# Performance work log

Measured on AMD Instinct MI355X. Metric: run time of the kernel, lower is better.

## Reference

```python
import jax, jax.numpy as jnp
import numpy as np

MARGIN = 0.3
EPS = 0.1              # label smoothing weight
NUM_CLASSES = 100000
WEIGHT_T = 1.0
WEIGHT_X = 1.0
BATCH = 1024
EMBED_DIM = 512


def setup_inputs() -> dict:
    key = jax.random.key(0)
    k1, k2, k3 = jax.random.split(key, 3)
    x = jax.random.normal(k1, (BATCH, EMBED_DIM), dtype=jnp.float32)
    # classifier: weight ~ N(0, 0.01), bias = 0 (matches nn.init in module)
    W = jax.random.normal(k2, (NUM_CLASSES, EMBED_DIM), dtype=jnp.float32) * 0.01
    b = jnp.zeros((NUM_CLASSES,), dtype=jnp.float32)
    labels = jax.random.randint(k3, (BATCH,), 0, NUM_CLASSES)
    return {"x": x, "W": W, "b": b, "labels": labels}


def reference(x, W, b, labels):
    # ---- TripletLoss with batch-hard mining ----
    sq = jnp.sum(x * x, axis=1)                      # [B]
    dist = sq[:, None] + sq[None, :] - 2.0 * (x @ x.T)  # [B, B]
    dist = jnp.sqrt(jnp.clip(dist, 1e-12))
    same = labels[:, None] == labels[None, :]        # [B, B] (diagonal True)
    dist_ap = jnp.max(jnp.where(same, dist, -jnp.inf), axis=1)  # hardest positive
    dist_an = jnp.min(jnp.where(same, jnp.inf, dist), axis=1)   # hardest negative
    # MarginRankingLoss(dist_an, dist_ap, y=1) = mean(relu(dist_ap - dist_an + margin))
    triplet_loss = jnp.mean(jnp.maximum(dist_ap - dist_an + MARGIN, 0.0))

    # ---- CrossEntropy with label smoothing ----
    logits = x @ W.T + b                              # [B, K]
    log_probs = jax.nn.log_softmax(logits, axis=1)
    onehot = jax.nn.one_hot(labels, NUM_CLASSES, dtype=log_probs.dtype)
    targets = (1.0 - EPS) * onehot + EPS / NUM_CLASSES
    ce_loss = jnp.sum(jnp.mean(-targets * log_probs, axis=0))

    return WEIGHT_T * triplet_loss + WEIGHT_X * ce_loss
```

## Files before the change

### kernel.cpp

```cpp
#include <hip/hip_runtime.h>
#include <hip/hip_bf16.h>
#include <math.h>

#define B 1024
#define D 512
#define KC 100000
#define MARGIN 0.3f
#define EPSSM 0.1f
#define NCP 782
#define NCP_PAD 784
#define NWREG (NCP_PAD * 8)

typedef __attribute__((ext_vector_type(8))) short bf16x8;
typedef __attribute__((ext_vector_type(4))) float f32x4;

__device__ __forceinline__ unsigned cvtpk(float lo, float hi) {
    union { __hip_bfloat162 h2; unsigned u; } cv;
    cv.h2 = __float22bfloat162_rn(make_float2(lo, hi));
    return cv.u;
}

__device__ __forceinline__ void async16(const void* g, void* l) {
    __builtin_amdgcn_global_load_lds((const __attribute__((address_space(1))) unsigned int*)g,
                                     (__attribute__((address_space(3))) unsigned int*)l,
                                     16, 0, 0);
}

#define VMCNT(n) asm volatile("s_waitcnt vmcnt(" #n ")" ::: "memory")
#define FENCE    asm volatile("" ::: "memory")


__global__ void init_ws(float* ws) {
    int i = blockIdx.x * blockDim.x + threadIdx.x;
    if (i < 2 * B) ws[i] = 0.f;
    else if (i < 3 * B) ((int*)ws)[i] = 0;
    else if (i < 4 * B) ((int*)ws)[i] = 0x7F800000;
}

__global__ __launch_bounds__(256) void prep_kernel(const float* __restrict__ x,
                                                   const float* __restrict__ W,
                                                   const float* __restrict__ bias,
                                                   const int* __restrict__ labels,
                                                   float* __restrict__ ws,
                                                   unsigned short* __restrict__ xp,
                                                   unsigned short* __restrict__ wp) {
    const int bid = blockIdx.x;
    const int tid = threadIdx.x;
    __shared__ float xs[8][D];
    __shared__ int labs[8];
    __shared__ float sqi[8];
    __shared__ float red_ap[8][4], red_an[8][4];

    if (bid >= 768) {
        size_t oid = (size_t)(bid - 768) * 256 + tid;
        int region = (int)(oid >> 10);
        int p = (int)(oid & 1023);
        int rloc = p >> 3;
        int ku = (p & 7) ^ (rloc & 7);
        int cp = region >> 3, kt = region & 7;
        int c = cp * 128 + rloc;
        unsigned pv[4];
        if (c < KC) {
            const float* src = W + (size_t)c * D + kt * 64 + ku * 8;
            f32x4 a = __builtin_nontemporal_load((const f32x4*)src);
            f32x4 b2 = __builtin_nontemporal_load((const f32x4*)(src + 4));
            pv[0] = cvtpk(a[0], a[1]);  pv[1] = cvtpk(a[2], a[3]);
            pv[2] = cvtpk(b2[0], b2[1]); pv[3] = cvtpk(b2[2], b2[3]);
        } else {
            pv[0] = pv[1] = pv[2] = pv[3] = 0u;
        }
        *(uint4*)(wp + ((size_t)region << 13) + (size_t)p * 8) = *(uint4*)pv;
        return;
    }
    if (bid >= 512) {
        int gid = (bid - 512) * 256 + tid;
        int row = gid >> 6;
        int rest = gid & 63;
        int kt = rest >> 3, ku = rest & 7;
        const float* src = x + (size_t)row * D + kt * 64 + ku * 8;
        f32x4 a = *(const f32x4*)src;
        f32x4 b2 = *(const f32x4*)(src + 4);
        unsigned pv[4] = { cvtpk(a[0], a[1]), cvtpk(a[2], a[3]), cvtpk(b2[0], b2[1]), cvtpk(b2[2], b2[3]) };
        size_t off = ((size_t)((row >> 7) * 8 + kt) << 13) + (size_t)((row & 127) * 8 + (ku ^ (row & 7))) * 8;
        *(uint4*)(xp + off) = *(uint4*)pv;
        return;
    }
    if (bid >= 256) {
        int wid = tid >> 6, lane = tid & 63;
        int row = (bid - 256) * 4 + wid;
        int lab = labels[row];
        const float* xr = x + (size_t)row * D;
        const float* wr = W + (size_t)lab * D;
        float dsum = 0.f;
#pragma unroll
        for (int u = 0; u < 2; ++u) {
            int k = (lane * 2 + u) * 4;
            float4 a = *(const float4*)&xr[k];
            float4 w = *(const float4*)&wr[k];
            dsum += a.x * w.x + a.y * w.y + a.z * w.z + a.w * w.w;
        }
        for (int o = 32; o >= 1; o >>= 1) dsum += __shfl_xor(dsum, o);
        if (lane == 0) atomicAdd(&ws[B + row], (1.f - EPSSM) * (dsum + bias[lab]));
        return;
    }

    const int row0 = (bid >> 1) * 8;
    const int jbase = (bid & 1) * 512;
    for (int f = tid; f < 8 * (D / 4); f += 256) {
        int r = f / (D / 4);
        int p = f % (D / 4);
        *(float4*)&xs[r][p * 4] = *(const float4*)&x[(size_t)(row0 + r) * D + p * 4];
    }
    if (tid < 8) labs[tid] = labels[row0 + tid];
    __syncthreads();
    if (tid < 8) {
        float s = 0.f;
        for (int k = 0; k < D; ++k) s += xs[tid][k] * xs[tid][k];
        sqi[tid] = s;
    }
    __syncthreads();

    float ap[8], an[8];
#pragma unroll
    for (int r = 0; r < 8; ++r) { ap[r] = -INFINITY; an[r] = INFINITY; }

    for (int j = jbase + tid; j < jbase + 512; j += 256) {
        int labj = labels[j];
        float dot[8];
        float sqj = 0.f;
#pragma unroll
        for (int r = 0; r < 8; ++r) dot[r] = 0.f;
        for (int kc = 0; kc < D; kc += 32) {
            float4 xj[8];
#pragma unroll
            for (int u = 0; u < 8; ++u) xj[u] = *(const float4*)&x[(size_t)j * D + kc + u * 4];
#pragma unroll
            for (int u = 0; u < 8; ++u)
                sqj += xj[u].x * xj[u].x + xj[u].y * xj[u].y + xj[u].z * xj[u].z + xj[u].w * xj[u].w;
#pragma unroll
            for (int r = 0; r < 8; ++r) {
                float d = 0.f;
#pragma unroll
                for (int u = 0; u < 8; ++u) {
                    const float4 a = *(const float4*)&xs[r][kc + u * 4];
                    d += a.x * xj[u].x + a.y * xj[u].y + a.z * xj[u].z + a.w * xj[u].w;
                }
                dot[r] += d;
            }
        }
#pragma unroll
        for (int r = 0; r < 8; ++r) {
            float d2 = sqi[r] + sqj - 2.f * dot[r];
            float dist = sqrtf(fmaxf(d2, 1e-12f));
            if (labj == labs[r]) ap[r] = fmaxf(ap[r], dist);
            else an[r] = fminf(an[r], dist);
        }
    }
#pragma unroll
    for (int r = 0; r < 8; ++r) {
        for (int o = 32; o >= 1; o >>= 1) {
            ap[r] = fmaxf(ap[r], __shfl_xor(ap[r], o));
            an[r] = fminf(an[r], __shfl_xor(an[r], o));
        }
    }
    int wid = tid >> 6;
    if ((tid & 63) == 0) {
#pragma unroll
        for (int r = 0; r < 8; ++r) { red_ap[r][wid] = ap[r]; red_an[r][wid] = an[r]; }
    }
    __syncthreads();
    if (tid < 8) {
        float a = -INFINITY, n = INFINITY;
#pragma unroll
        for (int w = 0; w < 4; ++w) { a = fmaxf(a, red_ap[tid][w]); n = fminf(n, red_an[tid][w]); }
        a = fmaxf(a, 0.f);
        int* apbits = (int*)(ws + 2 * B);
        int* anbits = (int*)(ws + 3 * B);
        atomicMax(&apbits[row0 + tid], __float_as_int(a));
        atomicMin(&anbits[row0 + tid], __float_as_int(n));
    }
}

__global__ __launch_bounds__(256, 2) void ce_gemm_k(const unsigned short* __restrict__ xp,
                                                    const unsigned short* __restrict__ wp,
                                                    const float* __restrict__ bias,
                                                    float* __restrict__ ws) {
    const int b = blockIdx.x;
    const int xcd = b & 7, slot = b >> 3;
    const int cp = (slot >> 3) * 8 + xcd;
    const int mb = slot & 7;
    if (cp >= NCP) return;
    const int rowbase = mb * 128;
    const int cbase = cp * 128;

    __shared__ unsigned short lds[32768];

    const int tid = threadIdx.x;
    const int lane = tid & 63;
    const int wid = tid >> 6;
    const int wm = wid >> 1, wn = wid & 1;
    const int q = lane >> 4, l15 = lane & 15;

    f32x4 acc[4][4];
#pragma unroll
    for (int m = 0; m < 4; ++m)
#pragma unroll
        for (int n = 0; n < 4; ++n) acc[m][n] = (f32x4){0.f, 0.f, 0.f, 0.f};

#define STAGE(kt_) {                                                               \
        unsigned short* lA = &lds[((kt_) & 1) * 16384];                            \
        unsigned short* lB = lA + 8192;                                            \
        const unsigned short* ga = xp + ((size_t)(mb * 8 + (kt_)) << 13);          \
        const unsigned short* gb = wp + ((size_t)(cp * 8 + (kt_)) << 13);          \
        _Pragma("unroll")                                                          \
        for (int i = 0; i < 4; ++i) {                                              \
            async16(ga + (i * 256 + tid) * 8, lA + (i * 256 + tid) * 8);           \
            async16(gb + (i * 256 + tid) * 8, lB + (i * 256 + tid) * 8);           \
        } }
#define READS(ks_, par_) {                                                         \
        const unsigned short* sA = &lds[(par_) * 16384];                           \
        const unsigned short* sB = sA + 8192;                                      \
        _Pragma("unroll") for (int m = 0; m < 4; ++m) {                            \
            int rl = wm * 64 + m * 16 + l15;                                       \
            af[m] = *(const bf16x8*)&sA[(rl * 8 + (((ks_) * 4 + q) ^ (rl & 7))) * 8]; } \
        _Pragma("unroll") for (int n = 0; n < 4; ++n) {                            \
            int rl = wn * 64 + n * 16 + l15;                                       \
            bfr[n] = *(const bf16x8*)&sB[(rl * 8 + (((ks_) * 4 + q) ^ (rl & 7))) * 8]; } }
#define MFMAC() {                                                                  \
        __builtin_amdgcn_s_setprio(1);                                             \
        _Pragma("unroll") for (int m = 0; m < 4; ++m)                              \
        _Pragma("unroll") for (int n = 0; n < 4; ++n)                              \
            acc[m][n] = __builtin_amdgcn_mfma_f32_16x16x32_bf16(                   \
                af[m], bfr[n], acc[m][n], 0, 0, 0);                                \
        __builtin_amdgcn_s_setprio(0); }

    STAGE(0); STAGE(1);

    bf16x8 af[4], bfr[4];
#pragma unroll
    for (int kt = 0; kt < 8; ++kt) {
        const int par = kt & 1;
        if (kt < 7) { VMCNT(8); } else { VMCNT(0); }
        __builtin_amdgcn_s_barrier(); FENCE;
        READS(0, par);
        MFMAC();
        READS(1, par);
        MFMAC();
        __builtin_amdgcn_s_barrier(); FENCE;
        if (kt + 2 < 8) STAGE(kt + 2);
    }
#undef STAGE
#undef READS
#undef MFMAC

    __syncthreads();
    float* redE = (float*)lds;
    float* redL = redE + 256;
    float biasv[4];
#pragma unroll
    for (int n = 0; n < 4; ++n) {
        int cc = cbase + wn * 64 + n * 16 + l15;
        biasv[n] = bias[cc < KC ? cc : KC - 1];
    }
#pragma unroll
    for (int m = 0; m < 4; ++m) {
#pragma unroll
        for (int r2 = 0; r2 < 4; ++r2) {
            float pe = 0.f, pl = 0.f;
#pragma unroll
            for (int n = 0; n < 4; ++n) {
                int cc = cbase + wn * 64 + n * 16 + l15;
                if (cc < KC) {
                    float lg = acc[m][n][r2] + biasv[n];
                    pe += __expf(lg);
                    pl += lg;
                }
            }
#pragma unroll
            for (int o = 1; o < 16; o <<= 1) {
                pe += __shfl_xor(pe, o);
                pl += __shfl_xor(pl, o);
            }
            if (l15 == 0) {
                int rowl = wm * 64 + m * 16 + q * 4 + r2;
                redE[rowl * 2 + wn] = pe;
                redL[rowl * 2 + wn] = pl;
            }
        }
    }
    __syncthreads();
    if (tid < 128) {
        float se = redE[tid * 2] + redE[tid * 2 + 1];
        float sl = redL[tid * 2] + redL[tid * 2 + 1];
        atomicAdd(&ws[rowbase + tid], se);
        atomicAdd(&ws[B + rowbase + tid], (EPSSM / (float)KC) * sl);
    }
}

__global__ __launch_bounds__(1024) void final_kernel(const float* __restrict__ ws,
                                                     float* __restrict__ out) {
    const float* sumexp = ws;
    const float* lin = ws + B;
    const int* apbits = (const int*)(ws + 2 * B);
    const int* anbits = (const int*)(ws + 3 * B);
    int i = threadIdx.x;
    float ce = logf(sumexp[i]) - lin[i];
    float ap = __int_as_float(apbits[i]);
    float an = __int_as_float(anbits[i]);
    float v = ce + fmaxf(ap - an + MARGIN, 0.f);
    for (int o = 32; o >= 1; o >>= 1) v += __shfl_xor(v, o);
    __shared__ float red[16];
    int wid = threadIdx.x >> 6, lane = threadIdx.x & 63;
    if (lane == 0) red[wid] = v;
    __syncthreads();
    if (threadIdx.x == 0) {
        float s = 0.f;
#pragma unroll
        for (int w = 0; w < 16; ++w) s += red[w];
        out[0] = s / (float)B;
    }
}

extern "C" void kernel_launch(void* const* d_in, const int* in_sizes, int n_in,
                              void* d_out, int out_size, void* d_ws, size_t ws_size,
                              hipStream_t stream) {
    const float* x = (const float*)d_in[0];
    const float* W = (const float*)d_in[1];
    const float* bias = (const float*)d_in[2];
    const int* labels = (const int*)d_in[3];
    float* out = (float*)d_out;
    float* ws = (float*)d_ws;

    unsigned short* xp = (unsigned short*)((char*)d_ws + 16384);
    unsigned short* wp = xp + (size_t)B * D;

    init_ws<<<16, 256, 0, stream>>>(ws);
    prep_kernel<<<768 + NWREG * 4, 256, 0, stream>>>(x, W, bias, labels, ws, xp, wp);
    ce_gemm_k<<<8 * NCP_PAD, 256, 0, stream>>>(xp, wp, bias, ws);
    final_kernel<<<1, 1024, 0, stream>>>(ws, out);
}
```

Before: 271.9 us.

## Load fp32 W directly into GEMM and convert to bf16 in-kernel

Removes the separate pass that converted the 100000x512 fp32 classifier weight into a swizzled bf16 copy. The GEMM now async-loads fp32 W tiles straight into LDS with K tiles of 32 instead of 64, and converts to bf16 when reading fragments. This avoids writing and re-reading a ~100MB intermediate, but each W tile is re-read by 8 row blocks in fp32, doubling the bytes per read unless L2 catches them. It also adds conversion ALU work and more barrier iterations in the inner loop. Smaller LDS allows occupancy 3.

```diff
diff --git a/kernel.cpp b/kernel.cpp
--- a/kernel.cpp
+++ b/kernel.cpp
@@ -9,7 +9,6 @@
 #define EPSSM 0.1f
 #define NCP 782
 #define NCP_PAD 784
-#define NWREG (NCP_PAD * 8)
 
 typedef __attribute__((ext_vector_type(8))) short bf16x8;
 typedef __attribute__((ext_vector_type(4))) float f32x4;
@@ -42,8 +41,7 @@
                                                    const float* __restrict__ bias,
                                                    const int* __restrict__ labels,
                                                    float* __restrict__ ws,
-                                                   unsigned short* __restrict__ xp,
-                                                   unsigned short* __restrict__ wp) {
+                                                   unsigned short* __restrict__ xp) {
     const int bid = blockIdx.x;
     const int tid = threadIdx.x;
     __shared__ float xs[8][D];
@@ -51,38 +49,18 @@
     __shared__ float sqi[8];
     __shared__ float red_ap[8][4], red_an[8][4];
 
-    if (bid >= 768) {
-        size_t oid = (size_t)(bid - 768) * 256 + tid;
-        int region = (int)(oid >> 10);
-        int p = (int)(oid & 1023);
-        int rloc = p >> 3;
-        int ku = (p & 7) ^ (rloc & 7);
-        int cp = region >> 3, kt = region & 7;
-        int c = cp * 128 + rloc;
-        unsigned pv[4];
-        if (c < KC) {
-            const float* src = W + (size_t)c * D + kt * 64 + ku * 8;
-            f32x4 a = __builtin_nontemporal_load((const f32x4*)src);
-            f32x4 b2 = __builtin_nontemporal_load((const f32x4*)(src + 4));
-            pv[0] = cvtpk(a[0], a[1]);  pv[1] = cvtpk(a[2], a[3]);
-            pv[2] = cvtpk(b2[0], b2[1]); pv[3] = cvtpk(b2[2], b2[3]);
-        } else {
-            pv[0] = pv[1] = pv[2] = pv[3] = 0u;
-        }
-        *(uint4*)(wp + ((size_t)region << 13) + (size_t)p * 8) = *(uint4*)pv;
-        return;
-    }
     if (bid >= 512) {
         int gid = (bid - 512) * 256 + tid;
-        int row = gid >> 6;
-        int rest = gid & 63;
-        int kt = rest >> 3, ku = rest & 7;
-        const float* src = x + (size_t)row * D + kt * 64 + ku * 8;
+        int region = gid >> 9;
+        int u = gid & 511;
+        int rloc = u >> 2, qpos = u & 3;
+        int ku = qpos ^ ((rloc >> 1) & 3);
+        int mb = region >> 4, kt = region & 15;
+        const float* src = x + (size_t)(mb * 128 + rloc) * D + kt * 32 + ku * 8;
         f32x4 a = *(const f32x4*)src;
         f32x4 b2 = *(const f32x4*)(src + 4);
         unsigned pv[4] = { cvtpk(a[0], a[1]), cvtpk(a[2], a[3]), cvtpk(b2[0], b2[1]), cvtpk(b2[2], b2[3]) };
-        size_t off = ((size_t)((row >> 7) * 8 + kt) << 13) + (size_t)((row & 127) * 8 + (ku ^ (row & 7))) * 8;
-        *(uint4*)(xp + off) = *(uint4*)pv;
+        *(uint4*)(xp + (size_t)region * 4096 + (size_t)u * 8) = *(uint4*)pv;
         return;
     }
     if (bid >= 256) {
@@ -181,8 +159,8 @@
     }
 }
 
-__global__ __launch_bounds__(256, 2) void ce_gemm_k(const unsigned short* __restrict__ xp,
-                                                    const unsigned short* __restrict__ wp,
+__global__ __launch_bounds__(256, 3) void ce_gemm_d(const unsigned short* __restrict__ xp,
+                                                    const float* __restrict__ W,
                                                     const float* __restrict__ bias,
                                                     float* __restrict__ ws) {
     const int b = blockIdx.x;
@@ -193,7 +171,7 @@
     const int rowbase = mb * 128;
     const int cbase = cp * 128;
 
-    __shared__ unsigned short lds[32768];
+    __shared__ unsigned short lds[24576];
 
     const int tid = threadIdx.x;
     const int lane = tid & 63;
@@ -208,24 +186,33 @@
         for (int n = 0; n < 4; ++n) acc[m][n] = (f32x4){0.f, 0.f, 0.f, 0.f};
 
 #define STAGE(kt_) {                                                               \
-        unsigned short* lA = &lds[((kt_) & 1) * 16384];                            \
-        unsigned short* lB = lA + 8192;                                            \
-        const unsigned short* ga = xp + ((size_t)(mb * 8 + (kt_)) << 13);          \
-        const unsigned short* gb = wp + ((size_t)(cp * 8 + (kt_)) << 13);          \
+        unsigned short* lA = &lds[((kt_) & 1) * 12288];                            \
+        float* lB = (float*)&lds[((kt_) & 1) * 12288 + 4096];                      \
+        const unsigned short* ga = xp + (size_t)(mb * 16 + (kt_)) * 4096;          \
+        async16(ga + tid * 8, lA + tid * 8);                                       \
+        async16(ga + 2048 + tid * 8, lA + 2048 + tid * 8);                         \
         _Pragma("unroll")                                                          \
         for (int i = 0; i < 4; ++i) {                                              \
-            async16(ga + (i * 256 + tid) * 8, lA + (i * 256 + tid) * 8);           \
-            async16(gb + (i * 256 + tid) * 8, lB + (i * 256 + tid) * 8);           \
+            int u = i * 256 + tid;                                                 \
+            int row = u >> 3;                                                      \
+            int lu = (u & 7) ^ (row & 7);                                          \
+            int rc = cbase + row; rc = rc < KC ? rc : KC - 1;                      \
+            async16(&W[(size_t)rc * D + (kt_) * 32 + lu * 4], lB + u * 4);         \
         } }
-#define READS(ks_, par_) {                                                         \
-        const unsigned short* sA = &lds[(par_) * 16384];                           \
-        const unsigned short* sB = sA + 8192;                                      \
+#define READS(par_) {                                                              \
+        const unsigned short* sA = &lds[(par_) * 12288];                           \
+        const float* sB = (const float*)&lds[(par_) * 12288 + 4096];               \
         _Pragma("unroll") for (int m = 0; m < 4; ++m) {                            \
             int rl = wm * 64 + m * 16 + l15;                                       \
-            af[m] = *(const bf16x8*)&sA[(rl * 8 + (((ks_) * 4 + q) ^ (rl & 7))) * 8]; } \
+            af[m] = *(const bf16x8*)&sA[(rl * 4 + (q ^ ((rl >> 1) & 3))) * 8]; }   \
         _Pragma("unroll") for (int n = 0; n < 4; ++n) {                            \
             int rl = wn * 64 + n * 16 + l15;                                       \
-            bfr[n] = *(const bf16x8*)&sB[(rl * 8 + (((ks_) * 4 + q) ^ (rl & 7))) * 8]; } }
+            f32x4 b0 = *(const f32x4*)&sB[rl * 32 + ((q * 2) ^ (rl & 7)) * 4];     \
+            f32x4 b1 = *(const f32x4*)&sB[rl * 32 + ((q * 2 + 1) ^ (rl & 7)) * 4]; \
+            union { unsigned u[4]; bf16x8 v; } cv;                                 \
+            cv.u[0] = cvtpk(b0[0], b0[1]); cv.u[1] = cvtpk(b0[2], b0[3]);          \
+            cv.u[2] = cvtpk(b1[0], b1[1]); cv.u[3] = cvtpk(b1[2], b1[3]);          \
+            bfr[n] = cv.v; } }
 #define MFMAC() {                                                                  \
         __builtin_amdgcn_s_setprio(1);                                             \
         _Pragma("unroll") for (int m = 0; m < 4; ++m)                              \
@@ -238,16 +225,14 @@
 
     bf16x8 af[4], bfr[4];
 #pragma unroll
-    for (int kt = 0; kt < 8; ++kt) {
+    for (int kt = 0; kt < 16; ++kt) {
         const int par = kt & 1;
-        if (kt < 7) { VMCNT(8); } else { VMCNT(0); }
+        if (kt < 15) { VMCNT(6); } else { VMCNT(0); }
         __builtin_amdgcn_s_barrier(); FENCE;
-        READS(0, par);
-        MFMAC();
-        READS(1, par);
+        READS(par);
         MFMAC();
         __builtin_amdgcn_s_barrier(); FENCE;
-        if (kt + 2 < 8) STAGE(kt + 2);
+        if (kt + 2 < 16) STAGE(kt + 2);
     }
 #undef STAGE
 #undef READS
@@ -332,10 +317,9 @@
     float* ws = (float*)d_ws;
 
     unsigned short* xp = (unsigned short*)((char*)d_ws + 16384);
-    unsigned short* wp = xp + (size_t)B * D;
 
     init_ws<<<16, 256, 0, stream>>>(ws);
-    prep_kernel<<<768 + NWREG * 4, 256, 0, stream>>>(x, W, bias, labels, ws, xp, wp);
-    ce_gemm_k<<<8 * NCP_PAD, 256, 0, stream>>>(xp, wp, bias, ws);
+    prep_kernel<<<768, 256, 0, stream>>>(x, W, bias, labels, ws, xp);
+    ce_gemm_d<<<8 * NCP_PAD, 256, 0, stream>>>(xp, W, bias, ws);
     final_kernel<<<1, 1024, 0, stream>>>(ws, out);
 }
```

After: 265.4 us. -2.4%, faster.
